# Optimization experiments

Hardware: AMD Instinct MI355X
Metric: run time of the kernel (lower is better)

## Reference

```python
import jax, jax.numpy as jnp
import numpy as np

NUM_ADD = 16
CD_W = 0.1
EPS = 1e-7


def setup_inputs() -> dict:
    key = jax.random.key(0)
    k1, k2 = jax.random.split(key)
    adv_pc = jax.random.normal(k1, (8, 2048, 3), dtype=jnp.float32)
    ori_pc = jax.random.normal(k2, (8, 8192, 3), dtype=jnp.float32)
    weights = jnp.ones((8,), dtype=jnp.float32)
    return {"adv_pc": adv_pc, "ori_pc": ori_pc, "weights": weights}


def _chamfer_adv2ori(adv, ori):
    # squared-L2 pairwise distances via the |a|^2 + |o|^2 - 2 a.o expansion
    a2 = jnp.sum(adv * adv, axis=-1)              # [B, K1]
    o2 = jnp.sum(ori * ori, axis=-1)              # [B, K2]
    cross = jnp.einsum('bkd,bmd->bkm', adv, ori)  # [B, K1, K2]
    d2 = jnp.maximum(a2[:, :, None] + o2[:, None, :] - 2.0 * cross, 0.0)
    return jnp.mean(jnp.min(d2, axis=2), axis=1)  # [B] loss1 (adv -> ori)


def _farthest_dist(clusters):
    # clusters: [B, num_add, P, 3]
    delta = clusters[:, :, None, :, :] - clusters[:, :, :, None, :] + EPS
    norm = jnp.linalg.norm(delta, axis=-1)        # [B, num_add, P, P]
    far = jnp.max(jnp.max(norm, axis=2), axis=2)  # [B, num_add]
    return jnp.sum(far, axis=1)                   # [B]


def reference(adv_pc, ori_pc, weights):
    B = adv_pc.shape[0]
    # chamfer (method='adv2ori', batch_avg=True)
    chamfer_loss = jnp.mean(_chamfer_adv2ori(adv_pc, ori_pc) * weights)
    # farthest pairwise dist per added cluster
    clusters = adv_pc.reshape(B, NUM_ADD, -1, 3)
    far_loss = jnp.mean(_farthest_dist(clusters) * weights)
    return far_loss + chamfer_loss * CD_W
```

## Files before the change

kernel.cpp:

```cpp
#include <hip/hip_runtime.h>
#include <float.h>
#include <math.h>

#define NB    8
#define K1    2048
#define K2    8192
#define NADD  16
#define PP    128
#define FEPS  1e-7f
#define CDW   0.1f

#define OQ     4
#define OQLEN  (K2 / OQ)
#define ABK    16
#define FAR_GRID 64
#define CH_GRID  (NB * OQ * ABK)
#define GRID_A   (FAR_GRID + CH_GRID)
#define RB_GRID  64

#define PMIN_OFF 0
#define PMIN_SZ  (OQ * NB * K1)
#define FARW_OFF PMIN_SZ
#define CHB_OFF  (FARW_OFF + NB * NADD)
#define CTR_OFF  (CHB_OFF + 64)

typedef __bf16 bf16x8 __attribute__((ext_vector_type(8)));
typedef float  f32x4  __attribute__((ext_vector_type(4)));
typedef unsigned long long u64;

__device__ __forceinline__ u64 bfbits(float x) {
    union { float f; unsigned int u; } c; c.f = x;
    unsigned int u = c.u;
    u += 0x7fffu + ((u >> 16) & 1u);
    return (u64)(u >> 16);
}

__global__ __launch_bounds__(256) void fused_a(const float* __restrict__ adv,
                                               const float* __restrict__ ori,
                                               float* __restrict__ pmins,
                                               float* __restrict__ far,
                                               unsigned int* __restrict__ ctr) {
    __shared__ u64 so[OQLEN];
    __shared__ float sred[4];
    const int bid = blockIdx.x;
    const int t   = threadIdx.x;
    if (bid == 0 && t == 0) *ctr = 0u;

    if (bid < FAR_GRID) {
        const int b  = bid >> 3;
        const int cp = bid & 7;
        const int g  = t >> 7;
        const int p  = t & 127;
        const int ci = cp * 2 + g;

        float* sf = (float*)so;
        const float* c = adv + (size_t)(b * K1 + ci * PP) * 3;
        float px = c[p * 3 + 0], py = c[p * 3 + 1], pz = c[p * 3 + 2];
        float* sx = sf + g * 384;
        sx[p] = px; sx[128 + p] = py; sx[256 + p] = pz;
        __syncthreads();

        const float pxm = px - FEPS, pym = py - FEPS, pzm = pz - FEPS;
        float mx = 0.f;
#pragma unroll 8
        for (int q = 0; q < PP; ++q) {
            float dx = sx[q] - pxm;
            float dy = sx[128 + q] - pym;
            float dz = sx[256 + q] - pzm;
            mx = fmaxf(mx, fmaf(dx, dx, fmaf(dy, dy, dz * dz)));
        }
#pragma unroll
        for (int off = 32; off; off >>= 1) mx = fmaxf(mx, __shfl_down(mx, off, 64));
        if ((t & 63) == 0) sred[t >> 6] = mx;
        __syncthreads();
        if (t == 0)   far[b * NADD + cp * 2 + 0] = sqrtf(fmaxf(sred[0], sred[1]));
        if (t == 128) far[b * NADD + cp * 2 + 1] = sqrtf(fmaxf(sred[2], sred[3]));
    } else {
        const int cb  = bid - FAR_GRID;
        const int abk = cb & 15;
        const int oq  = (cb >> 4) & 3;
        const int b   = cb >> 6;

#pragma unroll
        for (int i = 0; i < OQLEN / 256; ++i) {
            const int idx = i * 256 + t;
            const float* o = ori + ((size_t)b * K2 + oq * OQLEN + idx) * 3;
            float x = o[0], y = o[1], z = o[2];
            float o2 = fmaf(x, x, fmaf(y, y, z * z));
            so[idx] = bfbits(x) | (bfbits(y) << 16) | (bfbits(z) << 32)
                    | (bfbits(o2) << 48);
        }

        const int lane = t & 63;
        const int wv   = t >> 6;
        const int rowb = abk * 128 + wv * 32;
        const float* a0 = adv + ((size_t)b * K1 + rowb + (lane & 15)) * 3;
        const float* a1 = a0 + 48;
        const u64 q25 = 0x3e80ULL << 48;
        u64 pk0 = bfbits(-0.5f * a0[0]) | (bfbits(-0.5f * a0[1]) << 16)
                | (bfbits(-0.5f * a0[2]) << 32) | q25;
        u64 pk1 = bfbits(-0.5f * a1[0]) | (bfbits(-0.5f * a1[1]) << 16)
                | (bfbits(-0.5f * a1[2]) << 32) | q25;
        const bf16x8 af0 = __builtin_bit_cast(bf16x8, make_ulonglong2(pk0, 0ULL));
        const bf16x8 af1 = __builtin_bit_cast(bf16x8, make_ulonglong2(pk1, 0ULL));
        __syncthreads();

        const f32x4 z4 = {0.f, 0.f, 0.f, 0.f};
        f32x4 m0 = {FLT_MAX, FLT_MAX, FLT_MAX, FLT_MAX};
        f32x4 m1 = m0;
#pragma unroll 4
        for (int tl = 0; tl < OQLEN / 16; ++tl) {
            u64 lo = so[tl * 16 + (lane & 15)];
            bf16x8 bf = __builtin_bit_cast(bf16x8, make_ulonglong2(lo, 0ULL));
            f32x4 acc0 = __builtin_amdgcn_mfma_f32_16x16x32_bf16(af0, bf, z4, 0, 0, 0);
            f32x4 acc1 = __builtin_amdgcn_mfma_f32_16x16x32_bf16(af1, bf, z4, 0, 0, 0);
#pragma unroll
            for (int r = 0; r < 4; ++r) {
                m0[r] = fminf(m0[r], acc0[r]);
                m1[r] = fminf(m1[r], acc1[r]);
            }
        }

        float* pb = pmins + ((size_t)oq * NB + b) * K1 + rowb;
#pragma unroll
        for (int r = 0; r < 4; ++r) {
            float v0 = m0[r], v1 = m1[r];
#pragma unroll
            for (int msk = 1; msk < 16; msk <<= 1) {
                v0 = fminf(v0, __shfl_xor(v0, msk, 64));
                v1 = fminf(v1, __shfl_xor(v1, msk, 64));
            }
            if ((lane & 15) == 0) {
                const int rr = (lane >> 4) * 4 + r;
                pb[rr]      = v0;
                pb[16 + rr] = v1;
            }
        }
    }
}

__global__ __launch_bounds__(256) void reduce_b(const float* __restrict__ adv,
                                                const float* __restrict__ pmins,
                                                const float* __restrict__ far,
                                                const float* __restrict__ w,
                                                float* __restrict__ chbp,
                                                unsigned int* __restrict__ ctr,
                                                float* __restrict__ out) {
    __shared__ float s[4];
    __shared__ unsigned int lastflag;
    const int t  = threadIdx.x;
    const int kc = blockIdx.x & 7;
    const int b  = blockIdx.x >> 3;
    const int k  = kc * 256 + t;

    float m = FLT_MAX;
#pragma unroll
    for (int oq = 0; oq < OQ; ++oq)
        m = fminf(m, pmins[((size_t)oq * NB + b) * K1 + k]);

    const float* a = adv + (size_t)(b * K1 + k) * 3;
    float ax = a[0], ay = a[1], az = a[2];
    float a2 = fmaf(ax, ax, fmaf(ay, ay, az * az));
    float sum = fmaxf(a2 + m, 0.f);

#pragma unroll
    for (int off = 32; off; off >>= 1) sum += __shfl_down(sum, off, 64);
    const int lane = t & 63, wid = t >> 6;
    if (lane == 0) s[wid] = sum;
    __syncthreads();

    if (t == 0) {
        float part = s[0] + s[1] + s[2] + s[3];
        __hip_atomic_store(&chbp[b * 8 + kc], part,
                           __ATOMIC_RELEASE, __HIP_MEMORY_SCOPE_AGENT);
        unsigned int old = __hip_atomic_fetch_add(ctr, 1u,
                           __ATOMIC_ACQ_REL, __HIP_MEMORY_SCOPE_AGENT);
        lastflag = (old == RB_GRID - 1) ? 1u : 0u;
    }
    __syncthreads();
    if (!lastflag) return;

    float v = 0.f;
    if (t < 128) v = w[t >> 4] * far[t] * 0.125f;
    if (t < 64)
        v += (CDW * 0.125f / K1) * w[t >> 3] *
             __hip_atomic_load(&chbp[t], __ATOMIC_ACQUIRE, __HIP_MEMORY_SCOPE_AGENT);
#pragma unroll
    for (int off = 32; off; off >>= 1) v += __shfl_down(v, off, 64);
    __syncthreads();
    if (lane == 0) s[wid] = v;
    __syncthreads();
    if (t == 0) out[0] = s[0] + s[1] + s[2] + s[3];
}

extern "C" void kernel_launch(void* const* d_in, const int* in_sizes, int n_in,
                              void* d_out, int out_size, void* d_ws, size_t ws_size,
                              hipStream_t stream) {
    const float* adv = (const float*)d_in[0];
    const float* ori = (const float*)d_in[1];
    const float* w   = (const float*)d_in[2];
    float* ws    = (float*)d_ws;
    float* pmins = ws + PMIN_OFF;
    float* far   = ws + FARW_OFF;
    float* chbp  = ws + CHB_OFF;
    unsigned int* ctr = (unsigned int*)(ws + CTR_OFF);
    float* out   = (float*)d_out;

    fused_a<<<dim3(GRID_A), 256, 0, stream>>>(adv, ori, pmins, far, ctr);
    reduce_b<<<dim3(RB_GRID), 256, 0, stream>>>(adv, pmins, far, w, chbp, ctr, out);
}
```

Before: 22.66 us.

## Split ori across waves instead of blocks and reduce chamfer min in-block

New measurement: 22.34 us (median of 2 runs). Within noise of the previous version (-1.4%).

```diff
diff --git a/kernel.cpp b/kernel.cpp
--- a/kernel.cpp
+++ b/kernel.cpp
@@ -10,19 +10,14 @@
 #define FEPS  1e-7f
 #define CDW   0.1f
 
-#define OQ     4
-#define OQLEN  (K2 / OQ)
-#define ABK    16
+#define ABK      64
 #define FAR_GRID 64
-#define CH_GRID  (NB * OQ * ABK)
+#define CH_GRID  (NB * ABK)
 #define GRID_A   (FAR_GRID + CH_GRID)
-#define RB_GRID  64
+#define HPTS     4096
 
-#define PMIN_OFF 0
-#define PMIN_SZ  (OQ * NB * K1)
-#define FARW_OFF PMIN_SZ
-#define CHB_OFF  (FARW_OFF + NB * NADD)
-#define CTR_OFF  (CHB_OFF + 64)
+#define CHP_OFF  0
+#define FARW_OFF 512
 
 typedef __bf16 bf16x8 __attribute__((ext_vector_type(8)));
 typedef float  f32x4  __attribute__((ext_vector_type(4)));
@@ -34,17 +29,20 @@
     u += 0x7fffu + ((u >> 16) & 1u);
     return (u64)(u >> 16);
 }
+__device__ __forceinline__ u64 pack3(float x, float y, float z) {
+    float o2 = fmaf(x, x, fmaf(y, y, z * z));
+    return bfbits(x) | (bfbits(y) << 16) | (bfbits(z) << 32) | (bfbits(o2) << 48);
+}
 
 __global__ __launch_bounds__(256) void fused_a(const float* __restrict__ adv,
                                                const float* __restrict__ ori,
-                                               float* __restrict__ pmins,
-                                               float* __restrict__ far,
-                                               unsigned int* __restrict__ ctr) {
-    __shared__ u64 so[OQLEN];
+                                               float* __restrict__ chpart,
+                                               float* __restrict__ farw) {
+    __shared__ u64 so[HPTS];
+    __shared__ float smin[4][32];
     __shared__ float sred[4];
     const int bid = blockIdx.x;
     const int t   = threadIdx.x;
-    if (bid == 0 && t == 0) *ctr = 0u;
 
     if (bid < FAR_GRID) {
         const int b  = bid >> 3;
@@ -73,27 +71,16 @@
         for (int off = 32; off; off >>= 1) mx = fmaxf(mx, __shfl_down(mx, off, 64));
         if ((t & 63) == 0) sred[t >> 6] = mx;
         __syncthreads();
-        if (t == 0)   far[b * NADD + cp * 2 + 0] = sqrtf(fmaxf(sred[0], sred[1]));
-        if (t == 128) far[b * NADD + cp * 2 + 1] = sqrtf(fmaxf(sred[2], sred[3]));
+        if (t == 0)   farw[b * NADD + cp * 2 + 0] = sqrtf(fmaxf(sred[0], sred[1]));
+        if (t == 128) farw[b * NADD + cp * 2 + 1] = sqrtf(fmaxf(sred[2], sred[3]));
     } else {
-        const int cb  = bid - FAR_GRID;
-        const int abk = cb & 15;
-        const int oq  = (cb >> 4) & 3;
-        const int b   = cb >> 6;
-
-#pragma unroll
-        for (int i = 0; i < OQLEN / 256; ++i) {
-            const int idx = i * 256 + t;
-            const float* o = ori + ((size_t)b * K2 + oq * OQLEN + idx) * 3;
-            float x = o[0], y = o[1], z = o[2];
-            float o2 = fmaf(x, x, fmaf(y, y, z * z));
-            so[idx] = bfbits(x) | (bfbits(y) << 16) | (bfbits(z) << 32)
-                    | (bfbits(o2) << 48);
-        }
-
+        const int cb   = bid - FAR_GRID;
+        const int abk  = cb & (ABK - 1);
+        const int b    = cb >> 6;
         const int lane = t & 63;
         const int wv   = t >> 6;
-        const int rowb = abk * 128 + wv * 32;
+        const int rowb = abk * 32;
+
         const float* a0 = adv + ((size_t)b * K1 + rowb + (lane & 15)) * 3;
         const float* a1 = a0 + 48;
         const u64 q25 = 0x3e80ULL << 48;
@@ -103,25 +90,44 @@
                 | (bfbits(-0.5f * a1[2]) << 32) | q25;
         const bf16x8 af0 = __builtin_bit_cast(bf16x8, make_ulonglong2(pk0, 0ULL));
         const bf16x8 af1 = __builtin_bit_cast(bf16x8, make_ulonglong2(pk1, 0ULL));
-        __syncthreads();
 
         const f32x4 z4 = {0.f, 0.f, 0.f, 0.f};
         f32x4 m0 = {FLT_MAX, FLT_MAX, FLT_MAX, FLT_MAX};
         f32x4 m1 = m0;
+
+        for (int h = 0; h < 2; ++h) {
+            const float4* f4 = (const float4*)ori + ((size_t)b * 6144 + h * 3072);
+#pragma unroll
+            for (int i = 0; i < 4; ++i) {
+                const int pg = i * 256 + t;
+                float4 f0 = f4[pg * 3 + 0];
+                float4 f1 = f4[pg * 3 + 1];
+                float4 f2 = f4[pg * 3 + 2];
+                u64 w0 = pack3(f0.x, f0.y, f0.z);
+                u64 w1 = pack3(f0.w, f1.x, f1.y);
+                u64 w2 = pack3(f1.z, f1.w, f2.x);
+                u64 w3 = pack3(f2.y, f2.z, f2.w);
+                ulonglong2* dst = (ulonglong2*)&so[pg * 4];
+                dst[0] = make_ulonglong2(w0, w1);
+                dst[1] = make_ulonglong2(w2, w3);
+            }
+            __syncthreads();
+
 #pragma unroll 4
-        for (int tl = 0; tl < OQLEN / 16; ++tl) {
-            u64 lo = so[tl * 16 + (lane & 15)];
-            bf16x8 bf = __builtin_bit_cast(bf16x8, make_ulonglong2(lo, 0ULL));
-            f32x4 acc0 = __builtin_amdgcn_mfma_f32_16x16x32_bf16(af0, bf, z4, 0, 0, 0);
-            f32x4 acc1 = __builtin_amdgcn_mfma_f32_16x16x32_bf16(af1, bf, z4, 0, 0, 0);
+            for (int tl = 0; tl < 64; ++tl) {
+                u64 lo = so[wv * 1024 + tl * 16 + (lane & 15)];
+                bf16x8 bf = __builtin_bit_cast(bf16x8, make_ulonglong2(lo, 0ULL));
+                f32x4 acc0 = __builtin_amdgcn_mfma_f32_16x16x32_bf16(af0, bf, z4, 0, 0, 0);
+                f32x4 acc1 = __builtin_amdgcn_mfma_f32_16x16x32_bf16(af1, bf, z4, 0, 0, 0);
 #pragma unroll
-            for (int r = 0; r < 4; ++r) {
-                m0[r] = fminf(m0[r], acc0[r]);
-                m1[r] = fminf(m1[r], acc1[r]);
+                for (int r = 0; r < 4; ++r) {
+                    m0[r] = fminf(m0[r], acc0[r]);
+                    m1[r] = fminf(m1[r], acc1[r]);
+                }
             }
+            __syncthreads();
         }
 
-        float* pb = pmins + ((size_t)oq * NB + b) * K1 + rowb;
 #pragma unroll
         for (int r = 0; r < 4; ++r) {
             float v0 = m0[r], v1 = m1[r];
@@ -132,63 +138,40 @@
             }
             if ((lane & 15) == 0) {
                 const int rr = (lane >> 4) * 4 + r;
-                pb[rr]      = v0;
-                pb[16 + rr] = v1;
+                smin[wv][rr]      = v0;
+                smin[wv][16 + rr] = v1;
             }
+        }
+        __syncthreads();
+
+        if (t < 64) {
+            float sum = 0.f;
+            if (t < 32) {
+                float mm = fminf(fminf(smin[0][t], smin[1][t]),
+                                 fminf(smin[2][t], smin[3][t]));
+                const float* a = adv + ((size_t)b * K1 + rowb + t) * 3;
+                float a2 = fmaf(a[0], a[0], fmaf(a[1], a[1], a[2] * a[2]));
+                sum = fmaxf(a2 + mm, 0.f);
+            }
+#pragma unroll
+            for (int off = 32; off; off >>= 1) sum += __shfl_down(sum, off, 64);
+            if (t == 0) chpart[cb] = sum;
         }
     }
 }
 
-__global__ __launch_bounds__(256) void reduce_b(const float* __restrict__ adv,
-                                                const float* __restrict__ pmins,
-                                                const float* __restrict__ far,
-                                                const float* __restrict__ w,
-                                                float* __restrict__ chbp,
-                                                unsigned int* __restrict__ ctr,
-                                                float* __restrict__ out) {
+__global__ __launch_bounds__(256) void combine_b(const float* __restrict__ chpart,
+                                                 const float* __restrict__ farw,
+                                                 const float* __restrict__ w,
+                                                 float* __restrict__ out) {
     __shared__ float s[4];
-    __shared__ unsigned int lastflag;
-    const int t  = threadIdx.x;
-    const int kc = blockIdx.x & 7;
-    const int b  = blockIdx.x >> 3;
-    const int k  = kc * 256 + t;
-
-    float m = FLT_MAX;
-#pragma unroll
-    for (int oq = 0; oq < OQ; ++oq)
-        m = fminf(m, pmins[((size_t)oq * NB + b) * K1 + k]);
-
-    const float* a = adv + (size_t)(b * K1 + k) * 3;
-    float ax = a[0], ay = a[1], az = a[2];
-    float a2 = fmaf(ax, ax, fmaf(ay, ay, az * az));
-    float sum = fmaxf(a2 + m, 0.f);
-
-#pragma unroll
-    for (int off = 32; off; off >>= 1) sum += __shfl_down(sum, off, 64);
-    const int lane = t & 63, wid = t >> 6;
-    if (lane == 0) s[wid] = sum;
-    __syncthreads();
-
-    if (t == 0) {
-        float part = s[0] + s[1] + s[2] + s[3];
-        __hip_atomic_store(&chbp[b * 8 + kc], part,
-                           __ATOMIC_RELEASE, __HIP_MEMORY_SCOPE_AGENT);
-        unsigned int old = __hip_atomic_fetch_add(ctr, 1u,
-                           __ATOMIC_ACQ_REL, __HIP_MEMORY_SCOPE_AGENT);
-        lastflag = (old == RB_GRID - 1) ? 1u : 0u;
-    }
-    __syncthreads();
-    if (!lastflag) return;
-
-    float v = 0.f;
-    if (t < 128) v = w[t >> 4] * far[t] * 0.125f;
-    if (t < 64)
-        v += (CDW * 0.125f / K1) * w[t >> 3] *
-             __hip_atomic_load(&chbp[t], __ATOMIC_ACQUIRE, __HIP_MEMORY_SCOPE_AGENT);
+    const int t = threadIdx.x;
+    const float c1 = CDW * 0.125f / K1;
+    float v = c1 * (w[t >> 6] * chpart[t] + w[(t >> 6) + 4] * chpart[t + 256]);
+    if (t < 128) v += 0.125f * w[t >> 4] * farw[t];
 #pragma unroll
     for (int off = 32; off; off >>= 1) v += __shfl_down(v, off, 64);
-    __syncthreads();
-    if (lane == 0) s[wid] = v;
+    if ((t & 63) == 0) s[t >> 6] = v;
     __syncthreads();
     if (t == 0) out[0] = s[0] + s[1] + s[2] + s[3];
 }
@@ -199,13 +182,11 @@
     const float* adv = (const float*)d_in[0];
     const float* ori = (const float*)d_in[1];
     const float* w   = (const float*)d_in[2];
-    float* ws    = (float*)d_ws;
-    float* pmins = ws + PMIN_OFF;
-    float* far   = ws + FARW_OFF;
-    float* chbp  = ws + CHB_OFF;
-    unsigned int* ctr = (unsigned int*)(ws + CTR_OFF);
-    float* out   = (float*)d_out;
+    float* ws     = (float*)d_ws;
+    float* chpart = ws + CHP_OFF;
+    float* farw   = ws + FARW_OFF;
+    float* out    = (float*)d_out;
 
-    fused_a<<<dim3(GRID_A), 256, 0, stream>>>(adv, ori, pmins, far, ctr);
-    reduce_b<<<dim3(RB_GRID), 256, 0, stream>>>(adv, pmins, far, w, chbp, ctr, out);
+    fused_a<<<dim3(GRID_A), 256, 0, stream>>>(adv, ori, chpart, farw);
+    combine_b<<<dim3(1), 256, 0, stream>>>(chpart, farw, w, out);
 }
```
